# Kernel tuning notes

Measured on AMD Instinct MI355X. Metric: run time of the kernel, lower is better.

## Reference

```python
import jax, jax.numpy as jnp
import numpy as np

N_NODES = 100000
N_EDGES = 600000
D_IN = 128
D_OUT = 128


def setup_inputs() -> dict:
    key = jax.random.key(0)
    k1, k2, k3 = jax.random.split(key, 3)
    x = jax.random.normal(k1, (N_NODES, D_IN), dtype=jnp.float32)
    edge_index = jax.random.randint(k2, (2, N_EDGES), 0, N_NODES, dtype=jnp.int64)
    # Glorot-style init for the GCN weight, zero bias (PyG defaults)
    W = jax.random.normal(k3, (D_IN, D_OUT), dtype=jnp.float32) * (1.0 / np.sqrt(D_IN))
    b = jnp.zeros((D_OUT,), dtype=jnp.float32)
    return {"x": x, "edge_index": edge_index, "W": W, "b": b}


def reference(x, edge_index, W, b):
    """GCNConv: out = D^{-1/2} (A + I) D^{-1/2} (x @ W) + b."""
    n = x.shape[0]
    self_loop = jnp.arange(n, dtype=edge_index.dtype)
    src = jnp.concatenate([edge_index[0], self_loop])  # [E + N]
    dst = jnp.concatenate([edge_index[1], self_loop])

    xw = x @ W  # [N, D_OUT] dense transform before aggregation

    # symmetric normalization with self-loops
    deg = jax.ops.segment_sum(jnp.ones_like(dst, dtype=x.dtype), dst, num_segments=n)
    dinv = jnp.where(deg > 0, jax.lax.rsqrt(deg), 0.0)
    norm = dinv[src] * dinv[dst]  # [E + N]

    # gather source features, scale, scatter-add to destinations
    msgs = norm[:, None] * xw[src]  # [E + N, D_OUT]
    out = jax.ops.segment_sum(msgs, dst, num_segments=n)
    return out + b
```

## Files before the change

### kernel.cpp

```cpp
#include <hip/hip_runtime.h>
#include <hip/hip_bf16.h>
#include <stdint.h>

#define N_NODES 100000
#define N_EDGES 600000
#define D 128
#define WT_LD 136
#define NBLK ((N_NODES + 255) / 256)
#define CAP 32

typedef unsigned short u16;
typedef uint32_t u32;
typedef unsigned long long u64;
typedef __attribute__((ext_vector_type(8))) short bf16x8;
typedef __attribute__((ext_vector_type(4))) float f32x4;
typedef __attribute__((ext_vector_type(4))) int int4v;
typedef __attribute__((ext_vector_type(2))) int int2v;

union bfpack { bf16x8 v; u16 s[8]; };

__device__ __forceinline__ float bf2f(u16 u) {
    union { u32 i; float f; } v; v.i = ((u32)u) << 16; return v.f;
}
__device__ __forceinline__ u16 f2bf(float f) {
    union { float f; u32 i; } v; v.f = f;
    u32 lsb = (v.i >> 16) & 1u;
    return (u16)((v.i + 0x7fffu + lsb) >> 16);
}

__global__ __launch_bounds__(256) void k_init(const u32* __restrict__ xu,
                                              const int* __restrict__ ei,
                                              int* __restrict__ cnt,
                                              int* __restrict__ flags) {
    int t = threadIdx.x;
    int idx = blockIdx.x * 256 + t;
    if (idx < N_NODES) cnt[idx] = 0;
    if (blockIdx.x == 0) {
        __shared__ int c[2];
        if (t < 2) c[t] = 0;
        __syncthreads();
        const u32* eu = (const u32*)ei;
        int bad = 0, zc = 0;
        for (int i = 0; i < 16; i++) {
            u32 w = xu[t + 256 * i];
            int e0 = (w >> 7) & 0xFF, e1 = (w >> 23) & 0xFF;
            bad += ((e0 == 0 || e0 == 0xFF) ? 1 : 0) + ((e1 == 0 || e1 == 0xFF) ? 1 : 0);
            zc += (eu[2 * (t + 256 * i) + 1] == 0) ? 1 : 0;
        }
        atomicAdd(&c[0], bad);
        atomicAdd(&c[1], zc);
        __syncthreads();
        if (t == 0) { flags[0] = c[0] > 8 ? 1 : 0; flags[1] = c[1] > 2048 ? 1 : 0; }
    }
}

__global__ __launch_bounds__(256) void k_build(const int* __restrict__ ei,
                                               const int* __restrict__ flags,
                                               int* __restrict__ cnt,
                                               int* __restrict__ csr) {
    int t = blockIdx.x * 256 + threadIdx.x;
    if (2 * t >= N_EDGES) return;
    int s0, s1, d0, d1;
    if (flags[1]) {
        int4v sv = __builtin_nontemporal_load((const int4v*)(ei + 4 * t));
        int4v dv = __builtin_nontemporal_load((const int4v*)(ei + 2 * N_EDGES + 4 * t));
        s0 = sv.x; s1 = sv.z; d0 = dv.x; d1 = dv.z;
    } else {
        int2v sv = __builtin_nontemporal_load((const int2v*)(ei + 2 * t));
        int2v dv = __builtin_nontemporal_load((const int2v*)(ei + N_EDGES + 2 * t));
        s0 = sv.x; s1 = sv.y; d0 = dv.x; d1 = dv.y;
    }
    if ((unsigned)s0 >= N_NODES) s0 = 0;
    if ((unsigned)s1 >= N_NODES) s1 = 0;
    if ((unsigned)d0 >= N_NODES) d0 = 0;
    if ((unsigned)d1 >= N_NODES) d1 = 0;
    int slot0 = atomicAdd(&cnt[d0], 1);
    if (slot0 < CAP) csr[(long)d0 * CAP + slot0] = s0;
    int slot1 = atomicAdd(&cnt[d1], 1);
    if (slot1 < CAP) csr[(long)d1 * CAP + slot1] = s1;
}

__global__ __launch_bounds__(256) void k_gemm(const int* __restrict__ flags,
                                              const void* __restrict__ xp,
                                              const void* __restrict__ Wp,
                                              const int* __restrict__ deg,
                                              u16* __restrict__ xw) {
    __shared__ u16 Wt[128 * WT_LD];
    int t = threadIdx.x, wave = t >> 6, lane = t & 63;
    int m16 = lane & 15, q = lane >> 4;
    int row0 = blockIdx.x * 128 + wave * 32;
    int f32 = flags[0];
    f32x4 acc[2][8];
    for (int a = 0; a < 2; a++)
        for (int c = 0; c < 8; c++) acc[a][c] = (f32x4){0.f, 0.f, 0.f, 0.f};

    int r0 = row0 + m16;      if (r0 > N_NODES - 1) r0 = N_NODES - 1;
    int r1 = row0 + 16 + m16; if (r1 > N_NODES - 1) r1 = N_NODES - 1;

    if (f32) {
        const float* Wf = (const float*)Wp;
        const float* xf = (const float*)xp;
        for (int i = 0; i < 64; i++) {
            int idx = t + i * 256, k = idx >> 7, n = idx & 127;
            Wt[n * WT_LD + k] = f2bf(Wf[idx]);
        }
        __syncthreads();
        for (int kt = 0; kt < 4; kt++) {
            int kbase = kt * 32 + q * 8;
            f32x4 u0 = __builtin_nontemporal_load((const f32x4*)(xf + (long)r0 * D + kbase));
            f32x4 u1 = __builtin_nontemporal_load((const f32x4*)(xf + (long)r0 * D + kbase + 4));
            f32x4 v0 = __builtin_nontemporal_load((const f32x4*)(xf + (long)r1 * D + kbase));
            f32x4 v1 = __builtin_nontemporal_load((const f32x4*)(xf + (long)r1 * D + kbase + 4));
            float t0[8] = {u0.x, u0.y, u0.z, u0.w, u1.x, u1.y, u1.z, u1.w};
            float t1[8] = {v0.x, v0.y, v0.z, v0.w, v1.x, v1.y, v1.z, v1.w};
            bfpack h0, l0, h1, l1;
            for (int j = 0; j < 8; j++) {
                u16 a = f2bf(t0[j]); h0.s[j] = a; l0.s[j] = f2bf(t0[j] - bf2f(a));
                u16 b = f2bf(t1[j]); h1.s[j] = b; l1.s[j] = f2bf(t1[j] - bf2f(b));
            }
            for (int ct = 0; ct < 8; ct++) {
                bf16x8 bh = *(const bf16x8*)(&Wt[(ct * 16 + m16) * WT_LD + kbase]);
                acc[0][ct] = __builtin_amdgcn_mfma_f32_16x16x32_bf16(h0.v, bh, acc[0][ct], 0, 0, 0);
                acc[0][ct] = __builtin_amdgcn_mfma_f32_16x16x32_bf16(l0.v, bh, acc[0][ct], 0, 0, 0);
                acc[1][ct] = __builtin_amdgcn_mfma_f32_16x16x32_bf16(h1.v, bh, acc[1][ct], 0, 0, 0);
                acc[1][ct] = __builtin_amdgcn_mfma_f32_16x16x32_bf16(l1.v, bh, acc[1][ct], 0, 0, 0);
            }
        }
    } else {
        const u16* W16 = (const u16*)Wp;
        const u16* x16 = (const u16*)xp;
        for (int i = 0; i < 64; i++) {
            int idx = t + i * 256, k = idx >> 7, n = idx & 127;
            Wt[n * WT_LD + k] = W16[idx];
        }
        __syncthreads();
        for (int kt = 0; kt < 4; kt++) {
            int kbase = kt * 32 + q * 8;
            bf16x8 a0 = *(const bf16x8*)(x16 + (long)r0 * D + kbase);
            bf16x8 a1 = *(const bf16x8*)(x16 + (long)r1 * D + kbase);
            for (int ct = 0; ct < 8; ct++) {
                bf16x8 b = *(const bf16x8*)(&Wt[(ct * 16 + m16) * WT_LD + kbase]);
                acc[0][ct] = __builtin_amdgcn_mfma_f32_16x16x32_bf16(a0, b, acc[0][ct], 0, 0, 0);
                acc[1][ct] = __builtin_amdgcn_mfma_f32_16x16x32_bf16(a1, b, acc[1][ct], 0, 0, 0);
            }
        }
    }
    for (int a = 0; a < 2; a++)
        for (int r = 0; r < 4; r++) {
            int row = row0 + a * 16 + q * 4 + r;
            if (row < N_NODES) {
                float dr = rsqrtf((float)(deg[row] + 1));
                for (int ct = 0; ct < 8; ct++)
                    xw[(long)row * D + ct * 16 + m16] = f2bf(dr * acc[a][ct][r]);
            }
        }
}

__global__ __launch_bounds__(256) void k_agg(const int* __restrict__ flags,
                                             const u16* __restrict__ xw,
                                             const int* __restrict__ csr,
                                             const int* __restrict__ cnt,
                                             const void* __restrict__ bp,
                                             void* __restrict__ outp) {
    int wave = threadIdx.x >> 6, lane = threadIdx.x & 63;
    int n = blockIdx.x * 4 + wave;
    int c = lane * 2;
    int deg = cnt[n];
    float dn = rsqrtf((float)(deg + 1));
    int m = deg < CAP ? deg : CAP;
    const int* base = csr + (long)n * CAP;
    u32 pv = *(const u32*)(xw + (long)n * D + c);
    float ax = bf2f((u16)pv), ay = bf2f((u16)(pv >> 16));
    for (int j = 0; j < m; j += 8) {
        int4v qa = *(const int4v*)(base + j);
        int4v qb = *(const int4v*)(base + j + 4);
        bool v1 = (j + 1) < m, v2 = (j + 2) < m, v3 = (j + 3) < m;
        bool v4 = (j + 4) < m, v5 = (j + 5) < m, v6 = (j + 6) < m, v7 = (j + 7) < m;
        int s0 = qa.x;
        int s1 = v1 ? qa.y : n;
        int s2 = v2 ? qa.z : n;
        int s3 = v3 ? qa.w : n;
        int s4 = v4 ? qb.x : n;
        int s5 = v5 ? qb.y : n;
        int s6 = v6 ? qb.z : n;
        int s7 = v7 ? qb.w : n;
        u32 g0 = *(const u32*)(xw + (long)s0 * D + c);
        u32 g1 = *(const u32*)(xw + (long)s1 * D + c);
        u32 g2 = *(const u32*)(xw + (long)s2 * D + c);
        u32 g3 = *(const u32*)(xw + (long)s3 * D + c);
        u32 g4 = *(const u32*)(xw + (long)s4 * D + c);
        u32 g5 = *(const u32*)(xw + (long)s5 * D + c);
        u32 g6 = *(const u32*)(xw + (long)s6 * D + c);
        u32 g7 = *(const u32*)(xw + (long)s7 * D + c);
        ax += bf2f((u16)g0);            ay += bf2f((u16)(g0 >> 16));
        ax += v1 ? bf2f((u16)g1) : 0.f; ay += v1 ? bf2f((u16)(g1 >> 16)) : 0.f;
        ax += v2 ? bf2f((u16)g2) : 0.f; ay += v2 ? bf2f((u16)(g2 >> 16)) : 0.f;
        ax += v3 ? bf2f((u16)g3) : 0.f; ay += v3 ? bf2f((u16)(g3 >> 16)) : 0.f;
        ax += v4 ? bf2f((u16)g4) : 0.f; ay += v4 ? bf2f((u16)(g4 >> 16)) : 0.f;
        ax += v5 ? bf2f((u16)g5) : 0.f; ay += v5 ? bf2f((u16)(g5 >> 16)) : 0.f;
        ax += v6 ? bf2f((u16)g6) : 0.f; ay += v6 ? bf2f((u16)(g6 >> 16)) : 0.f;
        ax += v7 ? bf2f((u16)g7) : 0.f; ay += v7 ? bf2f((u16)(g7 >> 16)) : 0.f;
    }
    if (flags[0]) {
        const float* bf_ = (const float*)bp;
        float2 bb = *(const float2*)(bf_ + c);
        float* outf = (float*)outp;
        union { float2 f; u64 u; } o;
        o.f = make_float2(dn * ax + bb.x, dn * ay + bb.y);
        __builtin_nontemporal_store(o.u, (u64*)(outf + (long)n * D + c));
    } else {
        const u16* b16 = (const u16*)bp;
        u32 bb = *(const u32*)(b16 + c);
        u16* out16 = (u16*)outp;
        u32 o = (u32)f2bf(dn * ax + bf2f((u16)bb)) |
                ((u32)f2bf(dn * ay + bf2f((u16)(bb >> 16))) << 16);
        __builtin_nontemporal_store(o, (u32*)(out16 + (long)n * D + c));
    }
}

extern "C" void kernel_launch(void* const* d_in, const int* in_sizes, int n_in,
                              void* d_out, int out_size, void* d_ws, size_t ws_size,
                              hipStream_t stream) {
    const void* x  = d_in[0];
    const int* ei  = (const int*)d_in[1];
    const void* W  = d_in[2];
    const void* b  = d_in[3];
    char* ws = (char*)d_ws;

    int* flags = (int*)(ws + 0);
    int* cnt   = (int*)(ws + 64);
    int* csr   = (int*)(ws + 400128);
    u16* xw    = (u16*)(ws + 400128 + (size_t)N_NODES * CAP * 4);

    k_init<<<NBLK, 256, 0, stream>>>((const u32*)x, ei, cnt, flags);
    k_build<<<(N_EDGES / 2 + 255) / 256, 256, 0, stream>>>(ei, flags, cnt, csr);
    k_gemm<<<(N_NODES + 127) / 128, 256, 0, stream>>>(flags, x, W, cnt, xw);
    k_agg<<<N_NODES / 4, 256, 0, stream>>>(flags, xw, csr, cnt, b, d_out);
}
```

Measured before the change: 205.4 us.

## Pretranspose W in a prep kernel and read it from global in GEMM

Adds a small kernel that converts W to bf16 and transposes it once into workspace. The GEMM no longer stages W into shared memory per block; each wave now reads W fragments straight from global/L2. Each wave also handles 16 rows instead of 32, so the grid doubles. This removes the per-block W load, the conversion and the barrier, but it adds repeated global reads of W, lower reuse per wave, and one extra launch.

```diff
diff --git a/kernel.cpp b/kernel.cpp
--- a/kernel.cpp
+++ b/kernel.cpp
@@ -5,7 +5,6 @@
 #define N_NODES 100000
 #define N_EDGES 600000
 #define D 128
-#define WT_LD 136
 #define NBLK ((N_NODES + 255) / 256)
 #define CAP 32
 
@@ -54,6 +53,15 @@
     }
 }
 
+__global__ __launch_bounds__(256) void k_prep(const int* __restrict__ flags,
+                                              const void* __restrict__ Wp,
+                                              u16* __restrict__ Wt) {
+    int idx = blockIdx.x * 256 + threadIdx.x;
+    int k = idx >> 7, n = idx & 127;
+    u16 h = flags[0] ? f2bf(((const float*)Wp)[idx]) : ((const u16*)Wp)[idx];
+    Wt[n * D + k] = h;
+}
+
 __global__ __launch_bounds__(256) void k_build(const int* __restrict__ ei,
                                                const int* __restrict__ flags,
                                                int* __restrict__ cnt,
@@ -82,78 +90,53 @@
 
 __global__ __launch_bounds__(256) void k_gemm(const int* __restrict__ flags,
                                               const void* __restrict__ xp,
-                                              const void* __restrict__ Wp,
+                                              const u16* __restrict__ Wt,
                                               const int* __restrict__ deg,
                                               u16* __restrict__ xw) {
-    __shared__ u16 Wt[128 * WT_LD];
     int t = threadIdx.x, wave = t >> 6, lane = t & 63;
     int m16 = lane & 15, q = lane >> 4;
-    int row0 = blockIdx.x * 128 + wave * 32;
-    int f32 = flags[0];
-    f32x4 acc[2][8];
-    for (int a = 0; a < 2; a++)
-        for (int c = 0; c < 8; c++) acc[a][c] = (f32x4){0.f, 0.f, 0.f, 0.f};
-
-    int r0 = row0 + m16;      if (r0 > N_NODES - 1) r0 = N_NODES - 1;
-    int r1 = row0 + 16 + m16; if (r1 > N_NODES - 1) r1 = N_NODES - 1;
-
-    if (f32) {
-        const float* Wf = (const float*)Wp;
+    int row0 = (blockIdx.x * 4 + wave) * 16;
+    if (row0 >= N_NODES) return;
+    f32x4 acc[8];
+    for (int c = 0; c < 8; c++) acc[c] = (f32x4){0.f, 0.f, 0.f, 0.f};
+    int r0 = row0 + m16; if (r0 > N_NODES - 1) r0 = N_NODES - 1;
+
+    if (flags[0]) {
         const float* xf = (const float*)xp;
-        for (int i = 0; i < 64; i++) {
-            int idx = t + i * 256, k = idx >> 7, n = idx & 127;
-            Wt[n * WT_LD + k] = f2bf(Wf[idx]);
-        }
-        __syncthreads();
         for (int kt = 0; kt < 4; kt++) {
             int kbase = kt * 32 + q * 8;
             f32x4 u0 = __builtin_nontemporal_load((const f32x4*)(xf + (long)r0 * D + kbase));
             f32x4 u1 = __builtin_nontemporal_load((const f32x4*)(xf + (long)r0 * D + kbase + 4));
-            f32x4 v0 = __builtin_nontemporal_load((const f32x4*)(xf + (long)r1 * D + kbase));
-            f32x4 v1 = __builtin_nontemporal_load((const f32x4*)(xf + (long)r1 * D + kbase + 4));
-            float t0[8] = {u0.x, u0.y, u0.z, u0.w, u1.x, u1.y, u1.z, u1.w};
-            float t1[8] = {v0.x, v0.y, v0.z, v0.w, v1.x, v1.y, v1.z, v1.w};
-            bfpack h0, l0, h1, l1;
+            float tv[8] = {u0.x, u0.y, u0.z, u0.w, u1.x, u1.y, u1.z, u1.w};
+            bfpack h, l;
             for (int j = 0; j < 8; j++) {
-                u16 a = f2bf(t0[j]); h0.s[j] = a; l0.s[j] = f2bf(t0[j] - bf2f(a));
-                u16 b = f2bf(t1[j]); h1.s[j] = b; l1.s[j] = f2bf(t1[j] - bf2f(b));
+                u16 a = f2bf(tv[j]); h.s[j] = a; l.s[j] = f2bf(tv[j] - bf2f(a));
             }
             for (int ct = 0; ct < 8; ct++) {
-                bf16x8 bh = *(const bf16x8*)(&Wt[(ct * 16 + m16) * WT_LD + kbase]);
-                acc[0][ct] = __builtin_amdgcn_mfma_f32_16x16x32_bf16(h0.v, bh, acc[0][ct], 0, 0, 0);
-                acc[0][ct] = __builtin_amdgcn_mfma_f32_16x16x32_bf16(l0.v, bh, acc[0][ct], 0, 0, 0);
-                acc[1][ct] = __builtin_amdgcn_mfma_f32_16x16x32_bf16(h1.v, bh, acc[1][ct], 0, 0, 0);
-                acc[1][ct] = __builtin_amdgcn_mfma_f32_16x16x32_bf16(l1.v, bh, acc[1][ct], 0, 0, 0);
+                bf16x8 b = *(const bf16x8*)(Wt + (ct * 16 + m16) * D + kbase);
+                acc[ct] = __builtin_amdgcn_mfma_f32_16x16x32_bf16(h.v, b, acc[ct], 0, 0, 0);
+                acc[ct] = __builtin_amdgcn_mfma_f32_16x16x32_bf16(l.v, b, acc[ct], 0, 0, 0);
             }
         }
     } else {
-        const u16* W16 = (const u16*)Wp;
         const u16* x16 = (const u16*)xp;
-        for (int i = 0; i < 64; i++) {
-            int idx = t + i * 256, k = idx >> 7, n = idx & 127;
-            Wt[n * WT_LD + k] = W16[idx];
-        }
-        __syncthreads();
         for (int kt = 0; kt < 4; kt++) {
             int kbase = kt * 32 + q * 8;
-            bf16x8 a0 = *(const bf16x8*)(x16 + (long)r0 * D + kbase);
-            bf16x8 a1 = *(const bf16x8*)(x16 + (long)r1 * D + kbase);
+            bf16x8 a = *(const bf16x8*)(x16 + (long)r0 * D + kbase);
             for (int ct = 0; ct < 8; ct++) {
-                bf16x8 b = *(const bf16x8*)(&Wt[(ct * 16 + m16) * WT_LD + kbase]);
-                acc[0][ct] = __builtin_amdgcn_mfma_f32_16x16x32_bf16(a0, b, acc[0][ct], 0, 0, 0);
-                acc[1][ct] = __builtin_amdgcn_mfma_f32_16x16x32_bf16(a1, b, acc[1][ct], 0, 0, 0);
+                bf16x8 b = *(const bf16x8*)(Wt + (ct * 16 + m16) * D + kbase);
+                acc[ct] = __builtin_amdgcn_mfma_f32_16x16x32_bf16(a, b, acc[ct], 0, 0, 0);
             }
         }
     }
-    for (int a = 0; a < 2; a++)
-        for (int r = 0; r < 4; r++) {
-            int row = row0 + a * 16 + q * 4 + r;
-            if (row < N_NODES) {
-                float dr = rsqrtf((float)(deg[row] + 1));
-                for (int ct = 0; ct < 8; ct++)
-                    xw[(long)row * D + ct * 16 + m16] = f2bf(dr * acc[a][ct][r]);
-            }
-        }
+    for (int r = 0; r < 4; r++) {
+        int row = row0 + q * 4 + r;
+        if (row < N_NODES) {
+            float dr = rsqrtf((float)(deg[row] + 1));
+            for (int ct = 0; ct < 8; ct++)
+                xw[(long)row * D + ct * 16 + m16] = f2bf(dr * acc[ct][r]);
+        }
+    }
 }
 
 __global__ __launch_bounds__(256) void k_agg(const int* __restrict__ flags,
@@ -231,9 +214,11 @@
     int* cnt   = (int*)(ws + 64);
     int* csr   = (int*)(ws + 400128);
     u16* xw    = (u16*)(ws + 400128 + (size_t)N_NODES * CAP * 4);
+    u16* Wt    = (u16*)(ws + 38800128);
 
     k_init<<<NBLK, 256, 0, stream>>>((const u32*)x, ei, cnt, flags);
+    k_prep<<<64, 256, 0, stream>>>(flags, W, Wt);
     k_build<<<(N_EDGES / 2 + 255) / 256, 256, 0, stream>>>(ei, flags, cnt, csr);
-    k_gemm<<<(N_NODES + 127) / 128, 256, 0, stream>>>(flags, x, W, cnt, xw);
+    k_gemm<<<(N_NODES / 64) + 1, 256, 0, stream>>>(flags, x, Wt, cnt, xw);
     k_agg<<<N_NODES / 4, 256, 0, stream>>>(flags, xw, csr, cnt, b, d_out);
 }
```

Result: slower. 212.7 us (+3.6%).
